# Performance work log

Measured on AMD Instinct MI355X. Metric: run time of the kernel, lower is better.

The kernel has to match this reference:

```python
import jax, jax.numpy as jnp
import numpy as np

N = 50000
E = 800000
IN, H, OUT = 128, 96, 64
BN_EPS = 1e-5


def setup_inputs() -> dict:
    key = jax.random.key(0)
    ks = jax.random.split(key, 16)
    x = jax.random.normal(ks[0], (N, IN), dtype=jnp.float32)
    edge_index = jax.random.randint(ks[1], (2, E), 0, N, dtype=jnp.int64)
    edge_weight = jax.random.uniform(ks[2], (E,), dtype=jnp.float32)
    def lin(k, fo, fi):
        # PyG glorot-ish init
        s = 1.0 / np.sqrt(fi)
        return jax.random.uniform(k, (fo, fi), minval=-s, maxval=s, dtype=jnp.float32)
    W1, b1 = lin(ks[3], H, IN), jnp.zeros((H,), jnp.float32)
    W2, b2 = lin(ks[4], H, H), jnp.zeros((H,), jnp.float32)
    W3, b3 = lin(ks[5], OUT, H), jnp.zeros((OUT,), jnp.float32)
    g1 = jnp.ones((H,), jnp.float32); beta1 = jnp.zeros((H,), jnp.float32)
    m1 = 0.1 * jax.random.normal(ks[6], (H,), dtype=jnp.float32)
    v1 = jnp.abs(1.0 + 0.1 * jax.random.normal(ks[7], (H,), dtype=jnp.float32))
    g2 = jnp.ones((H,), jnp.float32); beta2 = jnp.zeros((H,), jnp.float32)
    m2 = 0.1 * jax.random.normal(ks[8], (H,), dtype=jnp.float32)
    v2 = jnp.abs(1.0 + 0.1 * jax.random.normal(ks[9], (H,), dtype=jnp.float32))
    return dict(x=x, edge_index=edge_index, edge_weight=edge_weight,
                W1=W1, b1=b1, W2=W2, b2=b2, W3=W3, b3=b3,
                g1=g1, beta1=beta1, m1=m1, v1=v1,
                g2=g2, beta2=beta2, m2=m2, v2=v2)


def gcn_norm(edge_index, edge_weight, n):
    # PyG gcn_norm with add_self_loops=True, fill_value=1.0
    loop = jnp.arange(n, dtype=edge_index.dtype)
    row = jnp.concatenate([edge_index[0], loop])  # sources
    col = jnp.concatenate([edge_index[1], loop])  # targets
    ew = jnp.concatenate([edge_weight, jnp.ones((n,), edge_weight.dtype)])
    deg = jax.ops.segment_sum(ew, col, num_segments=n)
    dis = jnp.where(deg > 0, jax.lax.rsqrt(deg), 0.0)  # inf -> 0 masked_fill
    norm = dis[row] * ew * dis[col]
    return row, col, norm


def gcn_conv(x, row, col, norm, W, b, n):
    xw = x @ W.T                       # [N, F_out] dense transform first
    msg = norm[:, None] * xw[row]      # [E+N, F_out] gather + edge scale
    out = jax.ops.segment_sum(msg, col, num_segments=n)  # scatter-add
    return out + b


def bn_eval(x, gamma, beta, mean, var):
    return (x - mean) * jax.lax.rsqrt(var + BN_EPS) * gamma + beta


def reference(x, edge_index, edge_weight, W1, b1, W2, b2, W3, b3,
              g1, beta1, m1, v1, g2, beta2, m2, v2):
    n = x.shape[0]
    row, col, norm = gcn_norm(edge_index, edge_weight, n)  # cached=True: shared
    h = gcn_conv(x, row, col, norm, W1, b1, n)
    h = jax.nn.relu(bn_eval(h, g1, beta1, m1, v1))
    h = gcn_conv(h, row, col, norm, W2, b2, n)
    h = jax.nn.relu(bn_eval(h, g2, beta2, m2, v2))
    out = gcn_conv(h, row, col, norm, W3, b3, n)
    return out
```

## Files before the change

kernel.cpp:

```cpp
#include <hip/hip_runtime.h>
#include <hip/hip_fp16.h>


constexpr float BN_EPS = 1e-5f;
constexpr float DEG_SCALE = 131072.0f;
constexpr float INV_DEG_SCALE = 1.0f / 131072.0f;
constexpr float NORM_SCALE = 32768.0f;
constexpr float INV_NORM_SCALE = 1.0f / 32768.0f;

typedef _Float16 f16x8 __attribute__((ext_vector_type(8)));
typedef float f32x4 __attribute__((ext_vector_type(4)));


template <int K, int F, bool F32X, bool F32W>
__device__ __forceinline__ void gemm_block(const void* __restrict__ Xin,
                                           const void* __restrict__ Win,
                                           _Float16* __restrict__ Y,
                                           int n0b, int tid, int n,
                                           _Float16* lds) {
    constexpr int KT = K / 32;
    constexpr int FT = F / 16;
    constexpr int LROW = (F == 96) ? 104 : 72;
    int wave = tid >> 6;
    int lane = tid & 63;
    int quad = lane >> 4;
    int r = lane & 15;
    int n0 = n0b + wave * 16;
    bool active = (n0 < n);

    if (active) {
        f16x8 a[KT];
        if (F32X) {
            const float* xr = (const float*)Xin + (size_t)(n0 + r) * K + quad * 8;
#pragma unroll
            for (int kt = 0; kt < KT; ++kt) {
                float4 v0 = *(const float4*)(xr + kt * 32);
                float4 v1 = *(const float4*)(xr + kt * 32 + 4);
                f16x8 t = {(_Float16)v0.x, (_Float16)v0.y, (_Float16)v0.z, (_Float16)v0.w,
                           (_Float16)v1.x, (_Float16)v1.y, (_Float16)v1.z, (_Float16)v1.w};
                a[kt] = t;
            }
        } else {
            const f16x8* xr = (const f16x8*)((const _Float16*)Xin + (size_t)(n0 + r) * K + quad * 8);
#pragma unroll
            for (int kt = 0; kt < KT; ++kt) a[kt] = xr[kt * 4];
        }

        f32x4 acc[FT];
#pragma unroll
        for (int ft = 0; ft < FT; ++ft) acc[ft] = (f32x4){0.f, 0.f, 0.f, 0.f};

#pragma unroll
        for (int kt = 0; kt < KT; ++kt) {
#pragma unroll
            for (int ft = 0; ft < FT; ++ft) {
                f16x8 b;
                if (F32W) {
                    const float* wr = (const float*)Win + (size_t)(ft * 16 + r) * K + kt * 32 + quad * 8;
                    float4 v0 = *(const float4*)wr;
                    float4 v1 = *(const float4*)(wr + 4);
                    f16x8 t = {(_Float16)v0.x, (_Float16)v0.y, (_Float16)v0.z, (_Float16)v0.w,
                               (_Float16)v1.x, (_Float16)v1.y, (_Float16)v1.z, (_Float16)v1.w};
                    b = t;
                } else {
                    b = *(const f16x8*)((const _Float16*)Win + (size_t)(ft * 16 + r) * K + kt * 32 + quad * 8);
                }
                acc[ft] = __builtin_amdgcn_mfma_f32_16x16x32_f16(a[kt], b, acc[ft], 0, 0, 0);
            }
        }

#pragma unroll
        for (int ft = 0; ft < FT; ++ft) {
#pragma unroll
            for (int reg = 0; reg < 4; ++reg) {
                int lr = wave * 16 + quad * 4 + reg;
                lds[(size_t)lr * LROW + ft * 16 + r] = (_Float16)acc[ft][reg];
            }
        }
    }
    __syncthreads();

    constexpr int CPR = F / 8;
    constexpr int TOTAL = 64 * CPR;
    for (int i = tid; i < TOTAL; i += 256) {
        int row = i / CPR, c = i - row * CPR;
        int grow = n0b + row;
        if (grow < n)
            *(uint4*)(Y + (size_t)grow * F + c * 8) =
                *(const uint4*)(lds + (size_t)row * LROW + c * 8);
    }
}


__global__ __launch_bounds__(256) void k_mega(
    const int* __restrict__ row_idx, const int* __restrict__ col_idx,
    const float* __restrict__ ew,
    unsigned long long* packed, unsigned char* rank, int e_cnt, int pair_b,
    int t1, int t2,
    const float* __restrict__ x, const float* __restrict__ W1,
    _Float16* __restrict__ bufA, int n,
    const float* __restrict__ W2, const float* __restrict__ W3,
    _Float16* __restrict__ w2h, _Float16* __restrict__ w3h,
    int w2n4, int w3n4) {
    __shared__ _Float16 lds[64 * 104];
    int b = blockIdx.x;
    if (b < 2 * pair_b) {
        int q = b >> 1;
        if ((b & 1) == 0) {
#pragma unroll
            for (int j = 0; j < 4; ++j) {
                int e = q * 1024 + j * 256 + (int)threadIdx.x;
                if (e < e_cnt) {
                    int c = col_idx[e];
                    int r = row_idx[e];
                    int t = (r >= t2) ? 2 : ((r >= t1) ? 1 : 0);
                    int sh = 24 + 10 * t;
                    unsigned wfix = (unsigned)(ew[e] * DEG_SCALE + 0.5f);
                    unsigned long long inc = (1ull << sh) | (unsigned long long)wfix;
                    unsigned long long old = atomicAdd(&packed[c], inc);
                    rank[e] = (unsigned char)((old >> sh) & 0x3FFull);
                }
            }
        } else {
            gemm_block<128, 96, true, true>(x, W1, bufA, q * 64, threadIdx.x, n, lds);
        }
    } else {
        int i = (b - 2 * pair_b) * 256 + (int)threadIdx.x;
        const float* src; _Float16* dst; int o;
        if (i < w2n4) { src = W2; dst = w2h; o = i; }
        else if (i < w2n4 + w3n4) { src = W3; dst = w3h; o = i - w2n4; }
        else return;
        float4 v = ((const float4*)src)[o];
        __half2 h0 = __floats2half2_rn(v.x, v.y);
        __half2 h1 = __floats2half2_rn(v.z, v.w);
        *(uint2*)(dst + (size_t)o * 4) = make_uint2(*(unsigned*)&h0, *(unsigned*)&h1);
    }
}


__device__ __forceinline__ int pk_cnt(unsigned long long p) {
    return (int)((p >> 24) & 0x3FF) + (int)((p >> 34) & 0x3FF) + (int)((p >> 44) & 0x3FF);
}

__global__ void k_scan1(const unsigned long long* __restrict__ packed,
                        int* bsum, float* dis, int n) {
    __shared__ int s[256];
    int i = blockIdx.x * 256 + threadIdx.x;
    int cnt = 0;
    if (i < n) {
        unsigned long long p = packed[i];
        cnt = pk_cnt(p);
        float wsum = (float)(unsigned)(p & 0xFFFFFFull) * INV_DEG_SCALE;
        dis[i] = rsqrtf(1.0f + wsum);
    }
    s[threadIdx.x] = cnt;
    __syncthreads();
    for (int off = 128; off > 0; off >>= 1) {
        if ((int)threadIdx.x < off) s[threadIdx.x] += s[threadIdx.x + off];
        __syncthreads();
    }
    if (threadIdx.x == 0) bsum[blockIdx.x] = s[0];
}

__global__ void k_scan23(const unsigned long long* __restrict__ packed,
                         const int* __restrict__ bsum,
                         int* row_ptr, int n, int e_total, int nb) {
    __shared__ int sb[256];
    __shared__ int s[256];
    int t = threadIdx.x;
    int bv = (t < nb) ? bsum[t] : 0;
    sb[t] = bv;
    __syncthreads();
    for (int off = 1; off < 256; off <<= 1) {
        int x = (t >= off) ? sb[t - off] : 0;
        __syncthreads();
        sb[t] += x;
        __syncthreads();
    }
    int boff = (blockIdx.x == 0) ? 0 : sb[blockIdx.x - 1];

    int i = blockIdx.x * 256 + t;
    int v = (i < n) ? pk_cnt(packed[i]) : 0;
    s[t] = v;
    __syncthreads();
    for (int off = 1; off < 256; off <<= 1) {
        int x = (t >= off) ? s[t - off] : 0;
        __syncthreads();
        s[t] += x;
        __syncthreads();
    }
    int ex = s[t] - v + boff;
    if (i < n) row_ptr[i] = ex;
    if (i == 0) row_ptr[n] = e_total;
}

__global__ void k_fill(const int* __restrict__ row_idx, const int* __restrict__ col_idx,
                       const float* __restrict__ ew, const float* __restrict__ dis,
                       const int* __restrict__ row_ptr, const unsigned char* __restrict__ rank,
                       const unsigned long long* __restrict__ packed,
                       unsigned* ep, int e_cnt, int t1, int t2) {
    int e = blockIdx.x * 256 + threadIdx.x;
    if (e < e_cnt) {
        int r = row_idx[e];
        int c = col_idx[e];
        unsigned long long p = packed[c];
        int c0 = (int)((p >> 24) & 0x3FF);
        int c1 = (int)((p >> 34) & 0x3FF);
        int t = (r >= t2) ? 2 : ((r >= t1) ? 1 : 0);
        int off = (t > 0 ? c0 : 0) + (t > 1 ? c1 : 0);
        float nm = dis[r] * ew[e];
        unsigned q = (unsigned)(nm * NORM_SCALE + 0.5f);
        if (q > 65535u) q = 65535u;
        ep[row_ptr[c] + off + (int)rank[e]] = ((unsigned)r << 16) | q;
    }
}


__device__ inline void cvt8(uint4 u, float* f) {
    float2 t;
    t = __half22float2(*(const __half2*)&u.x); f[0] = t.x; f[1] = t.y;
    t = __half22float2(*(const __half2*)&u.y); f[2] = t.x; f[3] = t.y;
    t = __half22float2(*(const __half2*)&u.z); f[4] = t.x; f[5] = t.y;
    t = __half22float2(*(const __half2*)&u.w); f[6] = t.x; f[7] = t.y;
}

__device__ inline void h8_acc(uint4 u, float w, float acc[8]) {
    float2 a = __half22float2(*(const __half2*)&u.x);
    float2 b = __half22float2(*(const __half2*)&u.y);
    float2 c = __half22float2(*(const __half2*)&u.z);
    float2 d = __half22float2(*(const __half2*)&u.w);
    acc[0] = fmaf(w, a.x, acc[0]); acc[1] = fmaf(w, a.y, acc[1]);
    acc[2] = fmaf(w, b.x, acc[2]); acc[3] = fmaf(w, b.y, acc[3]);
    acc[4] = fmaf(w, c.x, acc[4]); acc[5] = fmaf(w, c.y, acc[5]);
    acc[6] = fmaf(w, d.x, acc[6]); acc[7] = fmaf(w, d.y, acc[7]);
}

template <int FQ>
__device__ __forceinline__ void gather_row(const uint4* __restrict__ base,
                                           const unsigned* __restrict__ ep,
                                           int e0, int e1, int q, float acc[8]) {
    int e = e0;
    for (; e + 8 <= e1; e += 8) {
        unsigned p0 = ep[e + 0], p1 = ep[e + 1], p2 = ep[e + 2], p3 = ep[e + 3];
        unsigned p4 = ep[e + 4], p5 = ep[e + 5], p6 = ep[e + 6], p7 = ep[e + 7];
        uint4 x0 = base[(size_t)(p0 >> 16) * FQ + q];
        uint4 x1 = base[(size_t)(p1 >> 16) * FQ + q];
        uint4 x2 = base[(size_t)(p2 >> 16) * FQ + q];
        uint4 x3 = base[(size_t)(p3 >> 16) * FQ + q];
        uint4 x4 = base[(size_t)(p4 >> 16) * FQ + q];
        uint4 x5 = base[(size_t)(p5 >> 16) * FQ + q];
        uint4 x6 = base[(size_t)(p6 >> 16) * FQ + q];
        uint4 x7 = base[(size_t)(p7 >> 16) * FQ + q];
        h8_acc(x0, (float)(p0 & 0xffffu) * INV_NORM_SCALE, acc);
        h8_acc(x1, (float)(p1 & 0xffffu) * INV_NORM_SCALE, acc);
        h8_acc(x2, (float)(p2 & 0xffffu) * INV_NORM_SCALE, acc);
        h8_acc(x3, (float)(p3 & 0xffffu) * INV_NORM_SCALE, acc);
        h8_acc(x4, (float)(p4 & 0xffffu) * INV_NORM_SCALE, acc);
        h8_acc(x5, (float)(p5 & 0xffffu) * INV_NORM_SCALE, acc);
        h8_acc(x6, (float)(p6 & 0xffffu) * INV_NORM_SCALE, acc);
        h8_acc(x7, (float)(p7 & 0xffffu) * INV_NORM_SCALE, acc);
    }
    for (; e + 4 <= e1; e += 4) {
        unsigned p0 = ep[e + 0], p1 = ep[e + 1], p2 = ep[e + 2], p3 = ep[e + 3];
        uint4 x0 = base[(size_t)(p0 >> 16) * FQ + q];
        uint4 x1 = base[(size_t)(p1 >> 16) * FQ + q];
        uint4 x2 = base[(size_t)(p2 >> 16) * FQ + q];
        uint4 x3 = base[(size_t)(p3 >> 16) * FQ + q];
        h8_acc(x0, (float)(p0 & 0xffffu) * INV_NORM_SCALE, acc);
        h8_acc(x1, (float)(p1 & 0xffffu) * INV_NORM_SCALE, acc);
        h8_acc(x2, (float)(p2 & 0xffffu) * INV_NORM_SCALE, acc);
        h8_acc(x3, (float)(p3 & 0xffffu) * INV_NORM_SCALE, acc);
    }
    for (; e < e1; ++e) {
        unsigned p = ep[e];
        uint4 xv = base[(size_t)(p >> 16) * FQ + q];
        h8_acc(xv, (float)(p & 0xffffu) * INV_NORM_SCALE, acc);
    }
}


template <int FOUT>
__global__ __launch_bounds__(192) void k_aggr_mm(
    const _Float16* __restrict__ xw,
    const int* __restrict__ row_ptr, const unsigned* __restrict__ ep,
    const float* __restrict__ dis, const float* __restrict__ bias,
    const float* __restrict__ g, const float* __restrict__ beta,
    const float* __restrict__ m, const float* __restrict__ v,
    const _Float16* __restrict__ Wh,
    _Float16* __restrict__ Y, int n) {
    constexpr int LROW = 104;
    __shared__ _Float16 lds[16 * LROW];
    int tid = (int)threadIdx.x;
    int n0b = blockIdx.x * 16;
    int nl = tid / 12;
    int q = tid - nl * 12;
    int node = n0b + nl;
    const uint4* __restrict__ base = (const uint4*)xw;

    if (node < n) {
        float d = dis[node];
        float acc[8];
        {
            uint4 sv = base[(size_t)node * 12 + q];
            float t[8];
            cvt8(sv, t);
#pragma unroll
            for (int j = 0; j < 8; ++j) acc[j] = d * t[j];
        }
        gather_row<12>(base, ep, row_ptr[node], row_ptr[node + 1], q, acc);

        int fb = q * 8;
        const float4* bb = (const float4*)(bias + fb);
        float4 b0 = bb[0], b1 = bb[1];
        acc[0] = fmaf(acc[0], d, b0.x); acc[1] = fmaf(acc[1], d, b0.y);
        acc[2] = fmaf(acc[2], d, b0.z); acc[3] = fmaf(acc[3], d, b0.w);
        acc[4] = fmaf(acc[4], d, b1.x); acc[5] = fmaf(acc[5], d, b1.y);
        acc[6] = fmaf(acc[6], d, b1.z); acc[7] = fmaf(acc[7], d, b1.w);
#pragma unroll
        for (int j = 0; j < 8; ++j) {
            acc[j] = fmaxf((acc[j] - m[fb + j]) * rsqrtf(v[fb + j] + BN_EPS) * g[fb + j]
                           + beta[fb + j], 0.f);
        }
        __half2 h0 = __floats2half2_rn(acc[0], acc[1]);
        __half2 h1 = __floats2half2_rn(acc[2], acc[3]);
        __half2 h2 = __floats2half2_rn(acc[4], acc[5]);
        __half2 h3 = __floats2half2_rn(acc[6], acc[7]);
        *(uint4*)(lds + (size_t)nl * LROW + fb) =
            make_uint4(*(unsigned*)&h0, *(unsigned*)&h1, *(unsigned*)&h2, *(unsigned*)&h3);
    }
    __syncthreads();

    constexpr int FT = FOUT / 16;
    f32x4 cacc[FT];
    int lane = tid, quad = tid >> 4, r = tid & 15;
    if (tid < 64) {
        f16x8 a[3];
#pragma unroll
        for (int kt = 0; kt < 3; ++kt)
            a[kt] = *(const f16x8*)(lds + (size_t)r * LROW + kt * 32 + quad * 8);
#pragma unroll
        for (int ft = 0; ft < FT; ++ft) cacc[ft] = (f32x4){0.f, 0.f, 0.f, 0.f};
#pragma unroll
        for (int kt = 0; kt < 3; ++kt) {
#pragma unroll
            for (int ft = 0; ft < FT; ++ft) {
                f16x8 b = *(const f16x8*)(Wh + (size_t)(ft * 16 + r) * 96 + kt * 32 + quad * 8);
                cacc[ft] = __builtin_amdgcn_mfma_f32_16x16x32_f16(a[kt], b, cacc[ft], 0, 0, 0);
            }
        }
    }
    __syncthreads();
    if (tid < 64) {
#pragma unroll
        for (int ft = 0; ft < FT; ++ft) {
#pragma unroll
            for (int reg = 0; reg < 4; ++reg) {
                lds[(size_t)(quad * 4 + reg) * LROW + ft * 16 + r] = (_Float16)cacc[ft][reg];
            }
        }
    }
    (void)lane;
    __syncthreads();

    constexpr int CPR = FOUT / 8;
    for (int i = tid; i < 16 * CPR; i += 192) {
        int row = i / CPR, c = i - row * CPR;
        int grow = n0b + row;
        if (grow < n)
            *(uint4*)(Y + (size_t)grow * FOUT + c * 8) =
                *(const uint4*)(lds + (size_t)row * LROW + c * 8);
    }
}


__global__ __launch_bounds__(256) void k_aggr3(
    const _Float16* __restrict__ xw, const int* __restrict__ row_ptr,
    const unsigned* __restrict__ ep,
    const float* __restrict__ dis, const float* __restrict__ bias,
    float* __restrict__ out, int n) {
    constexpr int FQ = 8;
    int tg = blockIdx.x * 256 + threadIdx.x;
    int node = tg / FQ;
    int q = tg - node * FQ;
    if (node >= n) return;

    const uint4* __restrict__ base = (const uint4*)xw;
    float d = dis[node];
    float acc[8];
    {
        uint4 sv = base[(size_t)node * FQ + q];
        float t[8];
        cvt8(sv, t);
#pragma unroll
        for (int j = 0; j < 8; ++j) acc[j] = d * t[j];
    }
    gather_row<FQ>(base, ep, row_ptr[node], row_ptr[node + 1], q, acc);

    int fb = q * 8;
    const float4* bb = (const float4*)(bias + fb);
    float4 b0 = bb[0], b1 = bb[1];
    acc[0] = fmaf(acc[0], d, b0.x); acc[1] = fmaf(acc[1], d, b0.y);
    acc[2] = fmaf(acc[2], d, b0.z); acc[3] = fmaf(acc[3], d, b0.w);
    acc[4] = fmaf(acc[4], d, b1.x); acc[5] = fmaf(acc[5], d, b1.y);
    acc[6] = fmaf(acc[6], d, b1.z); acc[7] = fmaf(acc[7], d, b1.w);

    float* op = out + (size_t)node * 64 + fb;
    *(float4*)(op + 0) = make_float4(acc[0], acc[1], acc[2], acc[3]);
    *(float4*)(op + 4) = make_float4(acc[4], acc[5], acc[6], acc[7]);
}


extern "C" void kernel_launch(void* const* d_in, const int* in_sizes, int n_in,
                              void* d_out, int out_size, void* d_ws, size_t ws_size,
                              hipStream_t stream) {
    constexpr int IN = 128, H = 96, OUT = 64;

    const float* x   = (const float*)d_in[0];
    const int*   ei  = (const int*)d_in[1];
    const float* ew  = (const float*)d_in[2];
    const float* W1  = (const float*)d_in[3];
    const float* b1  = (const float*)d_in[4];
    const float* W2  = (const float*)d_in[5];
    const float* b2  = (const float*)d_in[6];
    const float* W3  = (const float*)d_in[7];
    const float* b3  = (const float*)d_in[8];
    const float* g1  = (const float*)d_in[9];
    const float* be1 = (const float*)d_in[10];
    const float* m1  = (const float*)d_in[11];
    const float* v1  = (const float*)d_in[12];
    const float* g2  = (const float*)d_in[13];
    const float* be2 = (const float*)d_in[14];
    const float* m2  = (const float*)d_in[15];
    const float* v2  = (const float*)d_in[16];

    const int N = in_sizes[0] / IN;
    const int E = in_sizes[2];
    const int* row_idx = ei;
    const int* col_idx = ei + E;
    const int T1 = N / 3, T2 = 2 * (N / 3);

    char* ws = (char*)d_ws;
    size_t off = 0;
    auto alloc = [&](size_t bytes) -> void* {
        void* p = ws + off;
        off = (off + bytes + 255) & ~(size_t)255;
        return p;
    };
    unsigned long long* packed = (unsigned long long*)alloc((size_t)N * 8);
    float*     dis     = (float*)alloc((size_t)N * 4);
    int*       row_ptr = (int*)alloc((size_t)(N + 1) * 4);
    int*       bsum    = (int*)alloc(256 * 4);
    unsigned char* rank = (unsigned char*)alloc((size_t)E);
    unsigned*  ep      = (unsigned*)alloc((size_t)E * 4);
    _Float16*  w2h     = (_Float16*)alloc((size_t)H * H * 2);
    _Float16*  w3h     = (_Float16*)alloc((size_t)OUT * H * 2);
    _Float16*  bufA    = (_Float16*)alloc((size_t)N * H * 2);
    _Float16*  bufB    = (_Float16*)alloc((size_t)N * H * 2);
    (void)ws_size; (void)n_in; (void)out_size;

    constexpr int W2N4 = H * H / 4, W3N4 = OUT * H / 4;
    const int NB = (N + 255) / 256;
    const int DEG1024 = (E + 1023) / 1024;
    const int GG = (N + 63) / 64;
    const int PAIR = (DEG1024 > GG) ? DEG1024 : GG;
    const int CVT_B = (W2N4 + W3N4 + 255) / 256;

    hipMemsetAsync(packed, 0, (size_t)N * 8, stream);
    k_mega<<<2 * PAIR + CVT_B, 256, 0, stream>>>(
        row_idx, col_idx, ew, packed, rank, E, PAIR, T1, T2,
        x, W1, bufA, N, W2, W3, w2h, w3h, W2N4, W3N4);
    k_scan1<<<NB, 256, 0, stream>>>(packed, bsum, dis, N);
    k_scan23<<<NB, 256, 0, stream>>>(packed, bsum, row_ptr, N, E, NB);
    k_fill<<<(E + 255) / 256, 256, 0, stream>>>(row_idx, col_idx, ew, dis,
                                                row_ptr, rank, packed, ep, E, T1, T2);

    const int GF = (N + 15) / 16;
    const int GA64 = ((size_t)N * (OUT / 8) + 255) / 256;

    k_aggr_mm<H><<<GF, 192, 0, stream>>>(
        bufA, row_ptr, ep, dis, b1, g1, be1, m1, v1, w2h, bufB, N);

    k_aggr_mm<OUT><<<GF, 192, 0, stream>>>(
        bufB, row_ptr, ep, dis, b2, g2, be2, m2, v2, w3h, bufA, N);

    k_aggr3<<<GA64, 256, 0, stream>>>(bufA, row_ptr, ep, dis, b3, (float*)d_out, N);
}
```

Before: 253.4 us.

## Quantize hidden features to int8 with per-row scales for gathers

The first two layers' transformed features are now stored as int8 with a per-row absmax scale instead of fp16. The aggregation kernels gather and dequantize them, folding the scale into the edge weight. This halves the bytes moved in the gather-heavy aggregation passes. In exchange it adds an LDS row-max reduction and a quantization step, extra scale loads per edge, and reduced numerical precision that could threaten tolerance.

```diff
diff --git a/kernel.cpp b/kernel.cpp
--- a/kernel.cpp
+++ b/kernel.cpp
@@ -12,85 +12,83 @@
 typedef float f32x4 __attribute__((ext_vector_type(4)));
 
 
-template <int K, int F, bool F32X, bool F32W>
-__device__ __forceinline__ void gemm_block(const void* __restrict__ Xin,
-                                           const void* __restrict__ Win,
-                                           _Float16* __restrict__ Y,
-                                           int n0b, int tid, int n,
-                                           _Float16* lds) {
-    constexpr int KT = K / 32;
-    constexpr int FT = F / 16;
-    constexpr int LROW = (F == 96) ? 104 : 72;
-    int wave = tid >> 6;
-    int lane = tid & 63;
-    int quad = lane >> 4;
-    int r = lane & 15;
+__device__ __forceinline__ void gemm1_q(const float* __restrict__ x,
+                                        const float* __restrict__ W1,
+                                        unsigned char* __restrict__ t1q,
+                                        float* __restrict__ scl1,
+                                        int n0b, int tid, int n,
+                                        _Float16* lds, unsigned* rmaxb) {
+    constexpr int LROW = 104;
+    if (tid < 64) rmaxb[tid] = 0u;
+    int wave = tid >> 6, lane = tid & 63, quad = lane >> 4, r = lane & 15;
     int n0 = n0b + wave * 16;
-    bool active = (n0 < n);
-
-    if (active) {
-        f16x8 a[KT];
-        if (F32X) {
-            const float* xr = (const float*)Xin + (size_t)(n0 + r) * K + quad * 8;
-#pragma unroll
-            for (int kt = 0; kt < KT; ++kt) {
-                float4 v0 = *(const float4*)(xr + kt * 32);
-                float4 v1 = *(const float4*)(xr + kt * 32 + 4);
-                f16x8 t = {(_Float16)v0.x, (_Float16)v0.y, (_Float16)v0.z, (_Float16)v0.w,
+    if (n0 < n) {
+        f16x8 a[4];
+        const float* xr = x + (size_t)(n0 + r) * 128 + quad * 8;
+#pragma unroll
+        for (int kt = 0; kt < 4; ++kt) {
+            float4 v0 = *(const float4*)(xr + kt * 32);
+            float4 v1 = *(const float4*)(xr + kt * 32 + 4);
+            f16x8 t = {(_Float16)v0.x, (_Float16)v0.y, (_Float16)v0.z, (_Float16)v0.w,
+                       (_Float16)v1.x, (_Float16)v1.y, (_Float16)v1.z, (_Float16)v1.w};
+            a[kt] = t;
+        }
+        f32x4 acc[6];
+#pragma unroll
+        for (int ft = 0; ft < 6; ++ft) acc[ft] = (f32x4){0.f, 0.f, 0.f, 0.f};
+#pragma unroll
+        for (int kt = 0; kt < 4; ++kt) {
+#pragma unroll
+            for (int ft = 0; ft < 6; ++ft) {
+                const float* wr = W1 + (size_t)(ft * 16 + r) * 128 + kt * 32 + quad * 8;
+                float4 v0 = *(const float4*)wr;
+                float4 v1 = *(const float4*)(wr + 4);
+                f16x8 b = {(_Float16)v0.x, (_Float16)v0.y, (_Float16)v0.z, (_Float16)v0.w,
                            (_Float16)v1.x, (_Float16)v1.y, (_Float16)v1.z, (_Float16)v1.w};
-                a[kt] = t;
-            }
-        } else {
-            const f16x8* xr = (const f16x8*)((const _Float16*)Xin + (size_t)(n0 + r) * K + quad * 8);
-#pragma unroll
-            for (int kt = 0; kt < KT; ++kt) a[kt] = xr[kt * 4];
-        }
-
-        f32x4 acc[FT];
-#pragma unroll
-        for (int ft = 0; ft < FT; ++ft) acc[ft] = (f32x4){0.f, 0.f, 0.f, 0.f};
-
-#pragma unroll
-        for (int kt = 0; kt < KT; ++kt) {
-#pragma unroll
-            for (int ft = 0; ft < FT; ++ft) {
-                f16x8 b;
-                if (F32W) {
-                    const float* wr = (const float*)Win + (size_t)(ft * 16 + r) * K + kt * 32 + quad * 8;
-                    float4 v0 = *(const float4*)wr;
-                    float4 v1 = *(const float4*)(wr + 4);
-                    f16x8 t = {(_Float16)v0.x, (_Float16)v0.y, (_Float16)v0.z, (_Float16)v0.w,
-                               (_Float16)v1.x, (_Float16)v1.y, (_Float16)v1.z, (_Float16)v1.w};
-                    b = t;
-                } else {
-                    b = *(const f16x8*)((const _Float16*)Win + (size_t)(ft * 16 + r) * K + kt * 32 + quad * 8);
-                }
                 acc[ft] = __builtin_amdgcn_mfma_f32_16x16x32_f16(a[kt], b, acc[ft], 0, 0, 0);
             }
         }
-
-#pragma unroll
-        for (int ft = 0; ft < FT; ++ft) {
-#pragma unroll
-            for (int reg = 0; reg < 4; ++reg) {
-                int lr = wave * 16 + quad * 4 + reg;
-                lds[(size_t)lr * LROW + ft * 16 + r] = (_Float16)acc[ft][reg];
-            }
-        }
-    }
-    __syncthreads();
-
-    constexpr int CPR = F / 8;
-    constexpr int TOTAL = 64 * CPR;
-    for (int i = tid; i < TOTAL; i += 256) {
-        int row = i / CPR, c = i - row * CPR;
+#pragma unroll
+        for (int ft = 0; ft < 6; ++ft)
+#pragma unroll
+            for (int reg = 0; reg < 4; ++reg)
+                lds[(size_t)(wave * 16 + quad * 4 + reg) * LROW + ft * 16 + r] =
+                    (_Float16)acc[ft][reg];
+    }
+    __syncthreads();
+    {
+        int row = tid >> 2, qt = tid & 3;
+        const _Float16* lp = lds + (size_t)row * LROW + qt * 24;
+        float mx = 0.f;
+#pragma unroll
+        for (int j = 0; j < 24; ++j) mx = fmaxf(mx, fabsf((float)lp[j]));
+        atomicMax(&rmaxb[row], __float_as_uint(mx));
+    }
+    __syncthreads();
+    for (int i = tid; i < 64 * 12; i += 256) {
+        int row = i / 12, c = i - row * 12;
         int grow = n0b + row;
-        if (grow < n)
-            *(uint4*)(Y + (size_t)grow * F + c * 8) =
-                *(const uint4*)(lds + (size_t)row * LROW + c * 8);
-    }
-}
-
+        if (grow >= n) continue;
+        float rm = __uint_as_float(rmaxb[row]);
+        float inv = (rm > 0.f) ? 127.0f / rm : 0.f;
+        const _Float16* lp = lds + (size_t)row * LROW + c * 8;
+        unsigned lo = 0, hi = 0;
+#pragma unroll
+        for (int j = 0; j < 4; ++j) {
+            int qv = __float2int_rn((float)lp[j] * inv);
+            qv = qv > 127 ? 127 : (qv < -127 ? -127 : qv);
+            lo |= ((unsigned)qv & 255u) << (8 * j);
+        }
+#pragma unroll
+        for (int j = 0; j < 4; ++j) {
+            int qv = __float2int_rn((float)lp[4 + j] * inv);
+            qv = qv > 127 ? 127 : (qv < -127 ? -127 : qv);
+            hi |= ((unsigned)qv & 255u) << (8 * j);
+        }
+        *(uint2*)(t1q + (size_t)grow * 96 + c * 8) = make_uint2(lo, hi);
+        if (c == 0) scl1[grow] = rm * (1.0f / 127.0f);
+    }
+}
 
 __global__ __launch_bounds__(256) void k_mega(
     const int* __restrict__ row_idx, const int* __restrict__ col_idx,
@@ -98,11 +96,12 @@
     unsigned long long* packed, unsigned char* rank, int e_cnt, int pair_b,
     int t1, int t2,
     const float* __restrict__ x, const float* __restrict__ W1,
-    _Float16* __restrict__ bufA, int n,
+    unsigned char* __restrict__ t1q, float* __restrict__ scl1, int n,
     const float* __restrict__ W2, const float* __restrict__ W3,
     _Float16* __restrict__ w2h, _Float16* __restrict__ w3h,
     int w2n4, int w3n4) {
     __shared__ _Float16 lds[64 * 104];
+    __shared__ unsigned rmaxb[64];
     int b = blockIdx.x;
     if (b < 2 * pair_b) {
         int q = b >> 1;
@@ -122,7 +121,7 @@
                 }
             }
         } else {
-            gemm_block<128, 96, true, true>(x, W1, bufA, q * 64, threadIdx.x, n, lds);
+            gemm1_q(x, W1, t1q, scl1, q * 64, (int)threadIdx.x, n, lds, rmaxb);
         }
     } else {
         int i = (b - 2 * pair_b) * 256 + (int)threadIdx.x;
@@ -233,6 +232,43 @@
     acc[2] = fmaf(w, b.x, acc[2]); acc[3] = fmaf(w, b.y, acc[3]);
     acc[4] = fmaf(w, c.x, acc[4]); acc[5] = fmaf(w, c.y, acc[5]);
     acc[6] = fmaf(w, d.x, acc[6]); acc[7] = fmaf(w, d.y, acc[7]);
+}
+
+__device__ inline void q8_acc(uint2 v, float ws, float acc[8]) {
+    int a = (int)v.x, b = (int)v.y;
+    acc[0] = fmaf(ws, (float)(int)(char)(a      ), acc[0]);
+    acc[1] = fmaf(ws, (float)(int)(char)(a >>  8), acc[1]);
+    acc[2] = fmaf(ws, (float)(int)(char)(a >> 16), acc[2]);
+    acc[3] = fmaf(ws, (float)(a >> 24),            acc[3]);
+    acc[4] = fmaf(ws, (float)(int)(char)(b      ), acc[4]);
+    acc[5] = fmaf(ws, (float)(int)(char)(b >>  8), acc[5]);
+    acc[6] = fmaf(ws, (float)(int)(char)(b >> 16), acc[6]);
+    acc[7] = fmaf(ws, (float)(b >> 24),            acc[7]);
+}
+
+__device__ __forceinline__ void gather_row_q(const unsigned char* __restrict__ tq,
+                                             const float* __restrict__ scl,
+                                             const unsigned* __restrict__ ep,
+                                             int e0, int e1, int q, float acc[8]) {
+    int e = e0;
+    for (; e + 4 <= e1; e += 4) {
+        unsigned p0 = ep[e + 0], p1 = ep[e + 1], p2 = ep[e + 2], p3 = ep[e + 3];
+        uint2 v0 = *(const uint2*)(tq + (size_t)(p0 >> 16) * 96 + q * 8);
+        uint2 v1 = *(const uint2*)(tq + (size_t)(p1 >> 16) * 96 + q * 8);
+        uint2 v2 = *(const uint2*)(tq + (size_t)(p2 >> 16) * 96 + q * 8);
+        uint2 v3 = *(const uint2*)(tq + (size_t)(p3 >> 16) * 96 + q * 8);
+        float s0 = scl[p0 >> 16], s1 = scl[p1 >> 16];
+        float s2 = scl[p2 >> 16], s3 = scl[p3 >> 16];
+        q8_acc(v0, (float)(p0 & 0xffffu) * INV_NORM_SCALE * s0, acc);
+        q8_acc(v1, (float)(p1 & 0xffffu) * INV_NORM_SCALE * s1, acc);
+        q8_acc(v2, (float)(p2 & 0xffffu) * INV_NORM_SCALE * s2, acc);
+        q8_acc(v3, (float)(p3 & 0xffffu) * INV_NORM_SCALE * s3, acc);
+    }
+    for (; e < e1; ++e) {
+        unsigned p = ep[e];
+        uint2 v = *(const uint2*)(tq + (size_t)(p >> 16) * 96 + q * 8);
+        q8_acc(v, (float)(p & 0xffffu) * INV_NORM_SCALE * scl[p >> 16], acc);
+    }
 }
 
 template <int FQ>
@@ -279,35 +315,35 @@
 }
 
 
-template <int FOUT>
+template <int FOUT, bool QOUT>
 __global__ __launch_bounds__(192) void k_aggr_mm(
-    const _Float16* __restrict__ xw,
+    const unsigned char* __restrict__ tq, const float* __restrict__ scl,
     const int* __restrict__ row_ptr, const unsigned* __restrict__ ep,
     const float* __restrict__ dis, const float* __restrict__ bias,
     const float* __restrict__ g, const float* __restrict__ beta,
     const float* __restrict__ m, const float* __restrict__ v,
     const _Float16* __restrict__ Wh,
-    _Float16* __restrict__ Y, int n) {
+    void* __restrict__ Yout, float* __restrict__ sclo, int n) {
     constexpr int LROW = 104;
     __shared__ _Float16 lds[16 * LROW];
+    __shared__ unsigned rmaxb[16];
     int tid = (int)threadIdx.x;
     int n0b = blockIdx.x * 16;
     int nl = tid / 12;
     int q = tid - nl * 12;
     int node = n0b + nl;
-    const uint4* __restrict__ base = (const uint4*)xw;
+    if (QOUT && tid < 16) rmaxb[tid] = 0u;
 
     if (node < n) {
         float d = dis[node];
         float acc[8];
+#pragma unroll
+        for (int j = 0; j < 8; ++j) acc[j] = 0.f;
         {
-            uint4 sv = base[(size_t)node * 12 + q];
-            float t[8];
-            cvt8(sv, t);
-#pragma unroll
-            for (int j = 0; j < 8; ++j) acc[j] = d * t[j];
-        }
-        gather_row<12>(base, ep, row_ptr[node], row_ptr[node + 1], q, acc);
+            uint2 sv = *(const uint2*)(tq + (size_t)node * 96 + q * 8);
+            q8_acc(sv, d * scl[node], acc);
+        }
+        gather_row_q(tq, scl, ep, row_ptr[node], row_ptr[node + 1], q, acc);
 
         int fb = q * 8;
         const float4* bb = (const float4*)(bias + fb);
@@ -332,7 +368,7 @@
 
     constexpr int FT = FOUT / 16;
     f32x4 cacc[FT];
-    int lane = tid, quad = tid >> 4, r = tid & 15;
+    int quad = tid >> 4, r = tid & 15;
     if (tid < 64) {
         f16x8 a[3];
 #pragma unroll
@@ -352,23 +388,57 @@
     __syncthreads();
     if (tid < 64) {
 #pragma unroll
-        for (int ft = 0; ft < FT; ++ft) {
-#pragma unroll
-            for (int reg = 0; reg < 4; ++reg) {
+        for (int ft = 0; ft < FT; ++ft)
+#pragma unroll
+            for (int reg = 0; reg < 4; ++reg)
                 lds[(size_t)(quad * 4 + reg) * LROW + ft * 16 + r] = (_Float16)cacc[ft][reg];
+    }
+    __syncthreads();
+
+    if (QOUT) {
+        if (tid < 64) {
+            int row = tid >> 2, qt = tid & 3;
+            const _Float16* lp = lds + (size_t)row * LROW + qt * 24;
+            float mx = 0.f;
+#pragma unroll
+            for (int j = 0; j < 24; ++j) mx = fmaxf(mx, fabsf((float)lp[j]));
+            atomicMax(&rmaxb[row], __float_as_uint(mx));
+        }
+        __syncthreads();
+        {
+            int row = nl, c = q;
+            int grow = n0b + row;
+            if (grow < n) {
+                float rm = __uint_as_float(rmaxb[row]);
+                float inv = (rm > 0.f) ? 127.0f / rm : 0.f;
+                const _Float16* lp = lds + (size_t)row * LROW + c * 8;
+                unsigned lo = 0, hi = 0;
+#pragma unroll
+                for (int j = 0; j < 4; ++j) {
+                    int qv = __float2int_rn((float)lp[j] * inv);
+                    qv = qv > 127 ? 127 : (qv < -127 ? -127 : qv);
+                    lo |= ((unsigned)qv & 255u) << (8 * j);
+                }
+#pragma unroll
+                for (int j = 0; j < 4; ++j) {
+                    int qv = __float2int_rn((float)lp[4 + j] * inv);
+                    qv = qv > 127 ? 127 : (qv < -127 ? -127 : qv);
+                    hi |= ((unsigned)qv & 255u) << (8 * j);
+                }
+                *(uint2*)((unsigned char*)Yout + (size_t)grow * 96 + c * 8) =
+                    make_uint2(lo, hi);
+                if (c == 0) sclo[grow] = rm * (1.0f / 127.0f);
             }
         }
-    }
-    (void)lane;
-    __syncthreads();
-
-    constexpr int CPR = FOUT / 8;
-    for (int i = tid; i < 16 * CPR; i += 192) {
-        int row = i / CPR, c = i - row * CPR;
-        int grow = n0b + row;
-        if (grow < n)
-            *(uint4*)(Y + (size_t)grow * FOUT + c * 8) =
-                *(const uint4*)(lds + (size_t)row * LROW + c * 8);
+    } else {
+        constexpr int CPR = FOUT / 8;
+        for (int i = tid; i < 16 * CPR; i += 192) {
+            int row = i / CPR, c = i - row * CPR;
+            int grow = n0b + row;
+            if (grow < n)
+                *(uint4*)((_Float16*)Yout + (size_t)grow * FOUT + c * 8) =
+                    *(const uint4*)(lds + (size_t)row * LROW + c * 8);
+        }
     }
 }
 
@@ -454,8 +524,11 @@
     unsigned*  ep      = (unsigned*)alloc((size_t)E * 4);
     _Float16*  w2h     = (_Float16*)alloc((size_t)H * H * 2);
     _Float16*  w3h     = (_Float16*)alloc((size_t)OUT * H * 2);
-    _Float16*  bufA    = (_Float16*)alloc((size_t)N * H * 2);
-    _Float16*  bufB    = (_Float16*)alloc((size_t)N * H * 2);
+    unsigned char* t1q = (unsigned char*)alloc((size_t)N * 96);
+    float*     scl1    = (float*)alloc((size_t)N * 4);
+    unsigned char* t2q = (unsigned char*)alloc((size_t)N * 96);
+    float*     scl2    = (float*)alloc((size_t)N * 4);
+    _Float16*  buf64   = (_Float16*)alloc((size_t)N * OUT * 2);
     (void)ws_size; (void)n_in; (void)out_size;
 
     constexpr int W2N4 = H * H / 4, W3N4 = OUT * H / 4;
@@ -468,7 +541,7 @@
     hipMemsetAsync(packed, 0, (size_t)N * 8, stream);
     k_mega<<<2 * PAIR + CVT_B, 256, 0, stream>>>(
         row_idx, col_idx, ew, packed, rank, E, PAIR, T1, T2,
-        x, W1, bufA, N, W2, W3, w2h, w3h, W2N4, W3N4);
+        x, W1, t1q, scl1, N, W2, W3, w2h, w3h, W2N4, W3N4);
     k_scan1<<<NB, 256, 0, stream>>>(packed, bsum, dis, N);
     k_scan23<<<NB, 256, 0, stream>>>(packed, bsum, row_ptr, N, E, NB);
     k_fill<<<(E + 255) / 256, 256, 0, stream>>>(row_idx, col_idx, ew, dis,
@@ -477,11 +550,11 @@
     const int GF = (N + 15) / 16;
     const int GA64 = ((size_t)N * (OUT / 8) + 255) / 256;
 
-    k_aggr_mm<H><<<GF, 192, 0, stream>>>(
-        bufA, row_ptr, ep, dis, b1, g1, be1, m1, v1, w2h, bufB, N);
-
-    k_aggr_mm<OUT><<<GF, 192, 0, stream>>>(
-        bufB, row_ptr, ep, dis, b2, g2, be2, m2, v2, w3h, bufA, N);
-
-    k_aggr3<<<GA64, 256, 0, stream>>>(bufA, row_ptr, ep, dis, b3, (float*)d_out, N);
-}
+    k_aggr_mm<H, true><<<GF, 192, 0, stream>>>(
+        t1q, scl1, row_ptr, ep, dis, b1, g1, be1, m1, v1, w2h, t2q, scl2, N);
+
+    k_aggr_mm<OUT, false><<<GF, 192, 0, stream>>>(
+        t2q, scl2, row_ptr, ep, dis, b2, g2, be2, m2, v2, w3h, buf64, nullptr, N);
+
+    k_aggr3<<<GA64, 256, 0, stream>>>(buf64, row_ptr, ep, dis, b3, (float*)d_out, N);
+}
```

New measurement: 243.9 us. -3.8%, faster.
